# Kernel optimization log

Measured on AMD Instinct MI355X. Metric: run time of the kernel, lower is better.

Reference implementation:

```python
import jax, jax.numpy as jnp
import numpy as np

EPS = 1e-5

def conv1x1(x, w, b):
    # x: (B,C,H,W), w: (O,C), b: (O,)
    return jnp.einsum('bchw,oc->bohw', x, w) + b[None, :, None, None]

def instance_norm(x):
    mu = jnp.mean(x, axis=(2, 3), keepdims=True)
    var = jnp.var(x, axis=(2, 3), keepdims=True)
    return (x - mu) / jnp.sqrt(var + EPS)

def setup_inputs() -> dict:
    key = jax.random.key(0)
    C = 256
    ks = jax.random.split(key, 16)
    def w(k):
        return jax.random.normal(k, (C, C), dtype=jnp.float32) * 0.02
    def b(k):
        return jax.random.normal(k, (C,), dtype=jnp.float32) * 0.01
    return {
        'x': jax.random.normal(ks[0], (8, C, 128, 128), dtype=jnp.float32),
        'wq1': w(ks[1]), 'bq1': b(ks[2]), 'wq2': w(ks[3]), 'bq2': b(ks[4]),
        'wk1': w(ks[5]), 'bk1': b(ks[6]), 'wk2': w(ks[7]), 'bk2': b(ks[8]),
        'wv': w(ks[9]), 'bv': b(ks[10]),
        'wg': w(ks[11]), 'bg': b(ks[12]),
        'wo': w(ks[13]), 'bo': b(ks[14]),
    }

def reference(x, wq1, bq1, wq2, bq2, wk1, bk1, wk2, bk2, wv, bv, wg, bg, wo, bo):
    head = 4
    B, C, H, W = x.shape
    c = C // head  # per-head channels
    n = H * W
    x = instance_norm(x)
    q = jax.nn.softplus(conv1x1(jax.nn.gelu(conv1x1(x, wq1, bq1), approximate=False), wq2, bq2))
    k = jax.nn.softplus(conv1x1(jax.nn.gelu(conv1x1(x, wk1, bk1), approximate=False), wk2, bk2))
    v = jax.nn.gelu(conv1x1(x, wv, bv), approximate=False)
    g = jax.nn.gelu(conv1x1(x, wg, bg), approximate=False)
    # b (head c) h w -> b head c (h w)
    q = q.reshape(B, head, c, n)
    kk = k.reshape(B, head, c, n)
    vv = v.reshape(B, head, c, n)
    kv = jnp.einsum('bhcn,bhdn->bhcd', kk, vv)  # (B,head,c,c)
    scale = 1.0 / jnp.sqrt(jnp.float32(c))
    z = jnp.einsum('bhcn,bhc->bhn', q, kk.sum(axis=-1)) * scale
    z = 1.0 / (z + jnp.float32(n))
    out = jnp.einsum('bhcn,bhcd->bhdn', q, kv) * scale
    out = (out + vv) * z[:, :, None, :]
    out = out.reshape(B, C, H, W)
    out = out * g
    return conv1x1(out, wo, bo)
```

## Files before the change

### kernel.cpp

```cpp
#include <hip/hip_runtime.h>
#include <stdint.h>

typedef short bf8 __attribute__((ext_vector_type(8)));
typedef short s4v __attribute__((ext_vector_type(4)));
typedef float f32x4 __attribute__((ext_vector_type(4)));

__device__ __forceinline__ short f2bf(float f){
  union { float f; unsigned u; } c; c.f = f;
  unsigned r = (c.u + 0x7fffu + ((c.u >> 16) & 1u)) >> 16;
  return (short)r;
}
__device__ __forceinline__ float bf2f(short s){
  union { unsigned u; float f; } c; c.u = ((unsigned)(unsigned short)s) << 16;
  return c.f;
}
__device__ __forceinline__ void gload16(const void* g, void* l){
  __builtin_amdgcn_global_load_lds((const __attribute__((address_space(1))) uint32_t*)g,
                                   (__attribute__((address_space(3))) uint32_t*)l, 16, 0, 0);
}
__device__ __forceinline__ float fast_erf(float x){
  const float s = fabsf(x);
  const float t = __builtin_amdgcn_rcpf(fmaf(0.3275911f, s, 1.0f));
  float p = fmaf(1.061405429f, t, -1.453152027f);
  p = fmaf(p, t, 1.421413741f);
  p = fmaf(p, t, -0.284496736f);
  p = fmaf(p, t, 0.254829592f);
  p = p * t;
  const float e = __expf(-s * s);
  return copysignf(fmaf(-p, e, 1.0f), x);
}
__device__ __forceinline__ float act_gelu(float x){
  return 0.5f * x * (1.0f + fast_erf(x * 0.70710678118654752f));
}
__device__ __forceinline__ float act_softplus(float x){
  const float e = __expf(-fabsf(x));
  return fmaxf(x, 0.0f) + __logf(1.0f + e);
}

__global__ __launch_bounds__(256) void k_statst(const float* __restrict__ x, short* __restrict__ xt,
                                                float* __restrict__ ps1, float* __restrict__ ps2){
  const int n0 = blockIdx.x * 64, c0 = blockIdx.y * 64, b = blockIdx.z;
  __shared__ short lt[64][68];
  const int t = threadIdx.x, nj = (t & 15) * 4, cb = t >> 4;
  float s1[4] = {0.f,0.f,0.f,0.f}, s2[4] = {0.f,0.f,0.f,0.f};
#pragma unroll
  for (int it = 0; it < 4; ++it){
    const int ci = cb + it * 16;
    const int row = b * 256 + c0 + ci;
    float4 v = *(const float4*)(x + (size_t)row * 16384 + n0 + nj);
    s4v o;
    o[0] = f2bf(v.x); o[1] = f2bf(v.y); o[2] = f2bf(v.z); o[3] = f2bf(v.w);
    *(s4v*)(&lt[ci][nj]) = o;
    s1[it] += v.x + v.y + v.z + v.w;
    s2[it] += v.x*v.x + v.y*v.y + v.z*v.z + v.w*v.w;
  }
  __syncthreads();
#pragma unroll
  for (int p = 0; p < 2; ++p){
    const int q = p * 256 + t;
    const int nl = q >> 3, c8 = (q & 7) * 8;
    bf8 o;
#pragma unroll
    for (int j = 0; j < 8; ++j) o[j] = lt[c8 + j][nl];
    *(bf8*)(xt + ((size_t)(b * 16384 + n0 + nl)) * 256 + c0 + c8) = o;
  }
#pragma unroll
  for (int it = 0; it < 4; ++it){
#pragma unroll
    for (int off = 8; off > 0; off >>= 1){
      s1[it] += __shfl_down(s1[it], off);
      s2[it] += __shfl_down(s2[it], off);
    }
  }
  if ((t & 15) == 0){
#pragma unroll
    for (int it = 0; it < 4; ++it){
      const int c = c0 + cb + it * 16;
      ps1[((size_t)(b * 256 + c)) * 256 + blockIdx.x] = s1[it];
      ps2[((size_t)(b * 256 + c)) * 256 + blockIdx.x] = s2[it];
    }
  }
}

__global__ __launch_bounds__(256) void k_red(const float* __restrict__ ps1, const float* __restrict__ ps2,
                                             float* __restrict__ mu, float* __restrict__ rsig){
  const int bc = blockIdx.x;
  const int t = threadIdx.x;
  __shared__ float a1[256], a2[256];
  a1[t] = ps1[(size_t)bc * 256 + t];
  a2[t] = ps2[(size_t)bc * 256 + t];
  __syncthreads();
  for (int s = 128; s > 0; s >>= 1){
    if (t < s){ a1[t] += a1[t+s]; a2[t] += a2[t+s]; }
    __syncthreads();
  }
  if (t == 0){
    float m = a1[0] * (1.0f/16384.0f);
    float v = a2[0] * (1.0f/16384.0f) - m*m;
    mu[bc] = m; rsig[bc] = rsqrtf(v + 1e-5f);
  }
}

__global__ __launch_bounds__(256) void k_norm(short* xn, const float* __restrict__ mu,
                                              const float* __restrict__ rsig){
  const int g = blockIdx.x * 256 + threadIdx.x;
#pragma unroll
  for (int pass = 0; pass < 8; ++pass){
    const int idx = g + pass * 524288;
    const int bn = idx >> 5, c8 = idx & 31;
    const int b = bn >> 14;
    const float* mp = mu + b * 256 + c8 * 8;
    const float* rp = rsig + b * 256 + c8 * 8;
    float4 m0 = *(const float4*)mp, m1 = *(const float4*)(mp + 4);
    float4 r0 = *(const float4*)rp, r1 = *(const float4*)(rp + 4);
    float mm[8] = {m0.x,m0.y,m0.z,m0.w,m1.x,m1.y,m1.z,m1.w};
    float rr[8] = {r0.x,r0.y,r0.z,r0.w,r1.x,r1.y,r1.z,r1.w};
    bf8 v = *(const bf8*)(xn + (size_t)idx * 8);
    bf8 o;
#pragma unroll
    for (int j = 0; j < 8; ++j) o[j] = f2bf((bf2f(v[j]) - mm[j]) * rr[j]);
    *(bf8*)(xn + (size_t)idx * 8) = o;
  }
}

__global__ __launch_bounds__(256) void k_wconv(const float* w0, const float* w1, const float* w2,
                                               const float* w3, const float* w4, const float* w5,
                                               const float* w6, short* __restrict__ wb){
  const int gid = blockIdx.x * 256 + threadIdx.x;
  const int mat = gid >> 14, r4 = gid & 16383;
  const float* srcs[7] = {w0, w1, w2, w3, w4, w5, w6};
  float4 v = *(const float4*)(srcs[mat] + (size_t)r4 * 4);
  s4v o; o[0] = f2bf(v.x); o[1] = f2bf(v.y); o[2] = f2bf(v.z); o[3] = f2bf(v.w);
  *(s4v*)(wb + (size_t)mat * 65536 + r4 * 4) = o;
}

template<int ACT>
__global__ __launch_bounds__(256, 2)
void k_gemm0(const short* __restrict__ A, const short* __restrict__ W,
             const float* __restrict__ bias, short* __restrict__ outp){
  __shared__ short sA[2][128 * 32];
  __shared__ short sB[2][256 * 32];
  const int t = threadIdx.x, l = t & 63, w = t >> 6;
  const int wr = w >> 1, wc = w & 1;
  const int lm = l & 15, lk = l >> 4;
  const size_t m0 = (size_t)blockIdx.x * 128;
  const int swz = ((lk ^ ((lm >> 1) & 3)) << 4);
  f32x4 acc[4][8] = {};

  auto stage = [&](int ks, int buf){
    const int k0 = ks * 32;
#pragma unroll
    for (int p = 0; p < 2; ++p){
      const int q = p * 256 + t, r = q >> 2, kc = q & 3;
      gload16(A + (m0 + r) * 256 + k0 + ((kc ^ ((r >> 1) & 3)) << 3),
              (char*)(&sA[buf][0]) + (p * 256 + w * 64) * 16);
    }
#pragma unroll
    for (int p = 0; p < 4; ++p){
      const int q = p * 256 + t, r = q >> 2, kc = q & 3;
      gload16(W + (size_t)r * 256 + k0 + ((kc ^ ((r >> 1) & 3)) << 3),
              (char*)(&sB[buf][0]) + (p * 256 + w * 64) * 16);
    }
  };

  stage(0, 0);
  __syncthreads();
  int cur = 0;
  for (int ks = 0; ks < 8; ++ks){
    if (ks < 7) stage(ks + 1, cur ^ 1);
    bf8 af[4], bfv[8];
#pragma unroll
    for (int mi = 0; mi < 4; ++mi)
      af[mi] = *(const bf8*)((const char*)(&sA[cur][0]) + (wr * 64 + mi * 16 + lm) * 64 + swz);
#pragma unroll
    for (int ni = 0; ni < 8; ++ni)
      bfv[ni] = *(const bf8*)((const char*)(&sB[cur][0]) + (wc * 128 + ni * 16 + lm) * 64 + swz);
#pragma unroll
    for (int mi = 0; mi < 4; ++mi)
#pragma unroll
      for (int ni = 0; ni < 8; ++ni)
        acc[mi][ni] = __builtin_amdgcn_mfma_f32_16x16x32_bf16(bfv[ni], af[mi], acc[mi][ni], 0, 0, 0);
    __syncthreads();
    cur ^= 1;
  }

#pragma unroll
  for (int ni = 0; ni < 8; ++ni){
    const int ob = wc * 128 + ni * 16 + lk * 4;
    const float4 b4 = *(const float4*)(bias + ob);
#pragma unroll
    for (int mi = 0; mi < 4; ++mi){
      const int px = wr * 64 + mi * 16 + lm;
      s4v o4;
#pragma unroll
      for (int j = 0; j < 4; ++j){
        float v = acc[mi][ni][j] + ((const float*)&b4)[j];
        if (ACT == 1) v = act_gelu(v);
        else if (ACT == 2) v = act_softplus(v);
        o4[j] = f2bf(v);
      }
      *(s4v*)(outp + (m0 + px) * 256 + ob) = o4;
    }
  }
}

__global__ __launch_bounds__(256, 2)
void k_chain(const short* __restrict__ A, const short* __restrict__ W1, const float* __restrict__ b1,
             const short* __restrict__ W2, const float* __restrict__ b2, short* __restrict__ out){
  __shared__ short sA[2][64 * 32];
  __shared__ short sB[2][256 * 32];
  __shared__ short h1[64 * 256];
  const int t = threadIdx.x, l = t & 63, w = t >> 6;
  const int lm = l & 15, lk = l >> 4;
  const size_t m0 = (size_t)blockIdx.x * 64;
  const int swz = ((lk ^ ((lm >> 1) & 3)) << 4);
  f32x4 acc[4][4] = {};

  auto stageA = [&](int ks, int buf){
    const int r = t >> 2, kc = t & 3;
    gload16(A + (m0 + r) * 256 + ks * 32 + ((kc ^ ((r >> 1) & 3)) << 3),
            (char*)(&sA[buf][0]) + w * 1024);
  };
  auto stageW = [&](const short* Wm, int ks, int buf){
#pragma unroll
    for (int p = 0; p < 4; ++p){
      const int q = p * 256 + t, r = q >> 2, kc = q & 3;
      gload16(Wm + (size_t)r * 256 + ks * 32 + ((kc ^ ((r >> 1) & 3)) << 3),
              (char*)(&sB[buf][0]) + (p * 256 + w * 64) * 16);
    }
  };

  stageA(0, 0); stageW(W1, 0, 0);
  __syncthreads();
  int cur = 0;
  for (int ks = 0; ks < 8; ++ks){
    if (ks < 7){ stageA(ks + 1, cur ^ 1); stageW(W1, ks + 1, cur ^ 1); }
    bf8 af[4], bfv[4];
#pragma unroll
    for (int mi = 0; mi < 4; ++mi)
      af[mi] = *(const bf8*)((const char*)(&sA[cur][0]) + (mi * 16 + lm) * 64 + swz);
#pragma unroll
    for (int ni = 0; ni < 4; ++ni)
      bfv[ni] = *(const bf8*)((const char*)(&sB[cur][0]) + (w * 64 + ni * 16 + lm) * 64 + swz);
#pragma unroll
    for (int mi = 0; mi < 4; ++mi)
#pragma unroll
      for (int ni = 0; ni < 4; ++ni)
        acc[mi][ni] = __builtin_amdgcn_mfma_f32_16x16x32_bf16(bfv[ni], af[mi], acc[mi][ni], 0, 0, 0);
    __syncthreads();
    cur ^= 1;
  }

  stageW(W2, 0, 0);
#pragma unroll
  for (int ni = 0; ni < 4; ++ni){
    const int ob = w * 64 + ni * 16 + lk * 4;
    const float4 b4 = *(const float4*)(b1 + ob);
#pragma unroll
    for (int mi = 0; mi < 4; ++mi){
      const int px = mi * 16 + lm;
      s4v o4;
#pragma unroll
      for (int j = 0; j < 4; ++j)
        o4[j] = f2bf(act_gelu(acc[mi][ni][j] + ((const float*)&b4)[j]));
      const int slot = (ob >> 3) ^ (px & 7);
      *(s4v*)((char*)h1 + px * 512 + (slot << 4) + (ob & 4) * 2) = o4;
      acc[mi][ni] = (f32x4){0.f, 0.f, 0.f, 0.f};
    }
  }
  __syncthreads();

  cur = 0;
  for (int ks = 0; ks < 8; ++ks){
    if (ks < 7) stageW(W2, ks + 1, cur ^ 1);
    bf8 af[4], bfv[4];
#pragma unroll
    for (int mi = 0; mi < 4; ++mi){
      const int row = mi * 16 + lm;
      const int slot = (ks * 4 + lk) ^ (row & 7);
      af[mi] = *(const bf8*)((const char*)h1 + row * 512 + (slot << 4));
    }
#pragma unroll
    for (int ni = 0; ni < 4; ++ni)
      bfv[ni] = *(const bf8*)((const char*)(&sB[cur][0]) + (w * 64 + ni * 16 + lm) * 64 + swz);
#pragma unroll
    for (int mi = 0; mi < 4; ++mi)
#pragma unroll
      for (int ni = 0; ni < 4; ++ni)
        acc[mi][ni] = __builtin_amdgcn_mfma_f32_16x16x32_bf16(bfv[ni], af[mi], acc[mi][ni], 0, 0, 0);
    __syncthreads();
    cur ^= 1;
  }
#pragma unroll
  for (int ni = 0; ni < 4; ++ni){
    const int ob = w * 64 + ni * 16 + lk * 4;
    const float4 b4 = *(const float4*)(b2 + ob);
#pragma unroll
    for (int mi = 0; mi < 4; ++mi){
      const int px = mi * 16 + lm;
      s4v o4;
#pragma unroll
      for (int j = 0; j < 4; ++j)
        o4[j] = f2bf(act_softplus(acc[mi][ni][j] + ((const float*)&b4)[j]));
      *(s4v*)(out + (m0 + px) * 256 + ob) = o4;
    }
  }
}

__global__ __launch_bounds__(256) void k_kv(const short* __restrict__ kg, const short* __restrict__ vg,
                                            float* __restrict__ kvpart, float* __restrict__ kspart){
  const int s = blockIdx.x, h = blockIdx.y, b = blockIdx.z;
  __shared__ short sk[64 * 72], sv[64 * 72];
  __shared__ float pl[256][8];
  const int t = threadIdx.x, l = t & 63, w = t >> 6;
  const int lm = l & 15, lk = l >> 4;
  float ksp[8];
#pragma unroll
  for (int j = 0; j < 8; ++j) ksp[j] = 0.f;
  f32x4 acc[4] = {};
  const size_t rowbase = ((size_t)b * 16384 + s * 2048) * 256 + h * 64;

  for (int tt = 0; tt < 32; ++tt){
    __syncthreads();
#pragma unroll
    for (int p = 0; p < 2; ++p){
      const int q = p * 256 + t;
      const int nl = q >> 3, c8 = (q & 7) * 8;
      bf8 kvv = *(const bf8*)(kg + rowbase + (size_t)(tt * 64 + nl) * 256 + c8);
      bf8 vvv = *(const bf8*)(vg + rowbase + (size_t)(tt * 64 + nl) * 256 + c8);
#pragma unroll
      for (int j = 0; j < 8; ++j){
        sk[(c8 + j) * 72 + nl] = kvv[j];
        sv[(c8 + j) * 72 + nl] = vvv[j];
        ksp[j] += bf2f(kvv[j]);
      }
    }
    __syncthreads();
#pragma unroll
    for (int ks = 0; ks < 2; ++ks){
      bf8 ak = *(const bf8*)((const char*)sk + (w * 16 + lm) * 144 + ks * 64 + lk * 16);
#pragma unroll
      for (int ni = 0; ni < 4; ++ni){
        bf8 bv = *(const bf8*)((const char*)sv + (ni * 16 + lm) * 144 + ks * 64 + lk * 16);
        acc[ni] = __builtin_amdgcn_mfma_f32_16x16x32_bf16(ak, bv, acc[ni], 0, 0, 0);
      }
    }
  }
#pragma unroll
  for (int j = 0; j < 8; ++j) pl[t][j] = ksp[j];
  __syncthreads();
  const size_t slot = (size_t)(b * 4 + h) * 8 + s;
  if (t < 64){
    float sum = 0.f;
    const int g8 = t >> 3, j = t & 7;
    for (int m = 0; m < 32; ++m) sum += pl[m * 8 + g8][j];
    kspart[slot * 64 + t] = sum;
  }
  float* kvp = kvpart + slot * 4096;
#pragma unroll
  for (int ni = 0; ni < 4; ++ni)
#pragma unroll
    for (int j = 0; j < 4; ++j){
      const int c = w * 16 + lk * 4 + j, d = ni * 16 + lm;
      kvp[c * 64 + d] = acc[ni][j];
    }
}

__global__ __launch_bounds__(256) void k_kvred(const float* __restrict__ kvpart, const float* __restrict__ kspart,
                                               short* __restrict__ kvT, float* __restrict__ ksum_s){
  const int gid = blockIdx.x * 256 + threadIdx.x;
#pragma unroll
  for (int i = 0; i < 8; ++i){
    const int o = gid * 8 + i;
    const int bh = o >> 12, rem = o & 4095, d = rem >> 6, c = rem & 63;
    float sum = 0.f;
#pragma unroll
    for (int s = 0; s < 8; ++s) sum += kvpart[((size_t)bh * 8 + s) * 4096 + c * 64 + d];
    kvT[o] = f2bf(sum * 0.125f);
  }
  if (gid < 2048){
    float sum = 0.f;
#pragma unroll
    for (int s = 0; s < 8; ++s) sum += kspart[((size_t)(gid >> 6) * 8 + s) * 64 + (gid & 63)];
    ksum_s[gid] = sum * 0.125f;
  }
}

__global__ __launch_bounds__(256, 2)
void k_fuse(const short* __restrict__ xn, const short* __restrict__ qg,
            const short* __restrict__ vg, const short* __restrict__ kvT,
            const float* __restrict__ ksum_s,
            const short* __restrict__ Wg, const float* __restrict__ bg,
            const short* __restrict__ Wo, const float* __restrict__ bo,
            float* __restrict__ outp){
  __shared__ short sA[2][64 * 32];
  __shared__ short sB[2][256 * 32];
  __shared__ short yl[64 * 256];
  __shared__ float sz[256];
  __shared__ float sks[256];
  const int t = threadIdx.x, l = t & 63, w = t >> 6;
  const int lm = l & 15, lk = l >> 4;
  const size_t m0 = (size_t)blockIdx.x * 64;
  const int b = (int)(m0 >> 14);
  const int h = w;
  const int swz = ((lk ^ ((lm >> 1) & 3)) << 4);

  sks[t] = ksum_s[b * 256 + t];

  auto stageA = [&](int ks, int buf){
    const int r = t >> 2, kc = t & 3;
    gload16(xn + (m0 + r) * 256 + ks * 32 + ((kc ^ ((r >> 1) & 3)) << 3),
            (char*)(&sA[buf][0]) + w * 1024);
  };
  auto stageW = [&](const short* Wm, int ks, int buf){
#pragma unroll
    for (int p = 0; p < 4; ++p){
      const int q = p * 256 + t, r = q >> 2, kc = q & 3;
      gload16(Wm + (size_t)r * 256 + ks * 32 + ((kc ^ ((r >> 1) & 3)) << 3),
              (char*)(&sB[buf][0]) + (p * 256 + w * 64) * 16);
    }
  };

  f32x4 acc[4][4] = {};

  stageA(0, 0); stageW(Wg, 0, 0);
  __syncthreads();
  int cur = 0;
  for (int ks = 0; ks < 8; ++ks){
    if (ks < 7){ stageA(ks + 1, cur ^ 1); stageW(Wg, ks + 1, cur ^ 1); }
    bf8 af[4], bfv[4];
#pragma unroll
    for (int mi = 0; mi < 4; ++mi)
      af[mi] = *(const bf8*)((const char*)(&sA[cur][0]) + (mi * 16 + lm) * 64 + swz);
#pragma unroll
    for (int ni = 0; ni < 4; ++ni)
      bfv[ni] = *(const bf8*)((const char*)(&sB[cur][0]) + (w * 64 + ni * 16 + lm) * 64 + swz);
#pragma unroll
    for (int mi = 0; mi < 4; ++mi)
#pragma unroll
      for (int ni = 0; ni < 4; ++ni)
        acc[mi][ni] = __builtin_amdgcn_mfma_f32_16x16x32_bf16(bfv[ni], af[mi], acc[mi][ni], 0, 0, 0);
    __syncthreads();
    cur ^= 1;
  }
  s4v g_pk[4][4];
#pragma unroll
  for (int ni = 0; ni < 4; ++ni){
    const int ob = h * 64 + ni * 16 + lk * 4;
    const float4 b4 = *(const float4*)(bg + ob);
#pragma unroll
    for (int mi = 0; mi < 4; ++mi){
#pragma unroll
      for (int j = 0; j < 4; ++j)
        g_pk[mi][ni][j] = f2bf(act_gelu(acc[mi][ni][j] + ((const float*)&b4)[j]));
      acc[mi][ni] = (f32x4){0.f, 0.f, 0.f, 0.f};
    }
  }

  {
    float dot = 0.f;
#pragma unroll
    for (int cc = 0; cc < 8; ++cc){
      bf8 qv = *(const bf8*)(qg + (m0 + l) * 256 + h * 64 + cc * 8);
#pragma unroll
      for (int j = 0; j < 8; ++j) dot += bf2f(qv[j]) * sks[h * 64 + cc * 8 + j];
    }
    sz[h * 64 + l] = 1.0f / (dot + 16384.0f);
  }

  const short* kvb = kvT + (size_t)b * 16384;
#pragma unroll
  for (int ks = 0; ks < 2; ++ks){
    bf8 aq[4];
#pragma unroll
    for (int mi = 0; mi < 4; ++mi)
      aq[mi] = *(const bf8*)(qg + (m0 + mi * 16 + lm) * 256 + h * 64 + ks * 32 + lk * 8);
#pragma unroll
    for (int ni = 0; ni < 4; ++ni){
      bf8 bk = *(const bf8*)(kvb + (size_t)(h * 64 + ni * 16 + lm) * 64 + ks * 32 + lk * 8);
#pragma unroll
      for (int mi = 0; mi < 4; ++mi)
        acc[mi][ni] = __builtin_amdgcn_mfma_f32_16x16x32_bf16(bk, aq[mi], acc[mi][ni], 0, 0, 0);
    }
  }
#pragma unroll
  for (int mi = 0; mi < 4; ++mi){
    const int px = mi * 16 + lm;
    const float zf = sz[h * 64 + px];
    const size_t base = (m0 + px) * 256;
#pragma unroll
    for (int ni = 0; ni < 4; ++ni){
      const int ch = h * 64 + ni * 16 + lk * 4;
      s4v v4 = *(const s4v*)(vg + base + ch);
      s4v o4;
#pragma unroll
      for (int j = 0; j < 4; ++j)
        o4[j] = f2bf((acc[mi][ni][j] + bf2f(v4[j])) * zf * bf2f(g_pk[mi][ni][j]));
      const int slot = (ch >> 3) ^ (px & 7);
      *(s4v*)((char*)yl + px * 512 + (slot << 4) + (ch & 4) * 2) = o4;
      acc[mi][ni] = (f32x4){0.f, 0.f, 0.f, 0.f};
    }
  }
  stageW(Wo, 0, 0);
  __syncthreads();

  cur = 0;
  for (int ks = 0; ks < 8; ++ks){
    if (ks < 7) stageW(Wo, ks + 1, cur ^ 1);
    bf8 af[4], bfv[4];
#pragma unroll
    for (int mi = 0; mi < 4; ++mi){
      const int row = mi * 16 + lm;
      const int slot = (ks * 4 + lk) ^ (row & 7);
      af[mi] = *(const bf8*)((const char*)yl + row * 512 + (slot << 4));
    }
#pragma unroll
    for (int ni = 0; ni < 4; ++ni)
      bfv[ni] = *(const bf8*)((const char*)(&sB[cur][0]) + (w * 64 + ni * 16 + lm) * 64 + swz);
#pragma unroll
    for (int mi = 0; mi < 4; ++mi)
#pragma unroll
      for (int ni = 0; ni < 4; ++ni)
        acc[mi][ni] = __builtin_amdgcn_mfma_f32_16x16x32_bf16(af[mi], bfv[ni], acc[mi][ni], 0, 0, 0);
    __syncthreads();
    cur ^= 1;
  }
  const int nb = (int)(m0 & 16383);
#pragma unroll
  for (int mi = 0; mi < 4; ++mi){
    const int np = nb + mi * 16 + lk * 4;
#pragma unroll
    for (int ni = 0; ni < 4; ++ni){
      const int o = w * 64 + ni * 16 + lm;
      const float bi = bo[o];
      float4 v;
      v.x = acc[mi][ni][0] + bi; v.y = acc[mi][ni][1] + bi;
      v.z = acc[mi][ni][2] + bi; v.w = acc[mi][ni][3] + bi;
      *(float4*)(outp + (((size_t)(b * 256 + o)) * 16384 + np)) = v;
    }
  }
}

extern "C" void kernel_launch(void* const* d_in, const int* in_sizes, int n_in,
                              void* d_out, int out_size, void* d_ws, size_t ws_size,
                              hipStream_t stream){
  (void)in_sizes; (void)n_in; (void)out_size; (void)ws_size;
  const float* x   = (const float*)d_in[0];
  const float* wq1 = (const float*)d_in[1];
  const float* bq1 = (const float*)d_in[2];
  const float* wq2 = (const float*)d_in[3];
  const float* bq2 = (const float*)d_in[4];
  const float* wk1 = (const float*)d_in[5];
  const float* bk1 = (const float*)d_in[6];
  const float* wk2 = (const float*)d_in[7];
  const float* bk2 = (const float*)d_in[8];
  const float* wv  = (const float*)d_in[9];
  const float* bv  = (const float*)d_in[10];
  const float* wg  = (const float*)d_in[11];
  const float* bg  = (const float*)d_in[12];
  const float* wo  = (const float*)d_in[13];
  const float* bo  = (const float*)d_in[14];

  char* ws = (char*)d_ws;
  float* mu     = (float*)(ws + 0);
  float* rsig   = (float*)(ws + 8192);
  short* wb     = (short*)(ws + 16384);
  float* kvpart = (float*)(ws + 933888);
  float* ps1    = (float*)(ws + 933888);
  float* ps2    = (float*)(ws + 3031040);
  float* kspart = (float*)(ws + 5128192);
  short* kvT    = (short*)(ws + 5193728);
  float* ksum_s = (float*)(ws + 5455872);
  short* B0 = (short*)(ws + 8388608);
  short* B1 = B0 + 33554432;
  short* B2 = B1 + 33554432;
  short* B3 = B2 + 33554432;

  k_wconv<<<448, 256, 0, stream>>>(wq1, wq2, wk1, wk2, wv, wg, wo, wb);
  k_statst<<<dim3(256, 4, 8), 256, 0, stream>>>(x, B0, ps1, ps2);
  k_red<<<2048, 256, 0, stream>>>(ps1, ps2, mu, rsig);
  k_norm<<<2048, 256, 0, stream>>>(B0, mu, rsig);
  k_chain<<<2048, 256, 0, stream>>>(B0, wb + 0 * 65536, bq1, wb + 1 * 65536, bq2, B2);
  k_chain<<<2048, 256, 0, stream>>>(B0, wb + 2 * 65536, bk1, wb + 3 * 65536, bk2, B3);
  k_gemm0<1><<<1024, 256, 0, stream>>>(B0, wb + 4 * 65536, bv, B1);
  k_kv<<<dim3(8, 4, 8), 256, 0, stream>>>(B3, B1, kvpart, kspart);
  k_kvred<<<64, 256, 0, stream>>>(kvpart, kspart, kvT, ksum_s);
  k_fuse<<<2048, 256, 0, stream>>>(B0, B2, B1, kvT, ksum_s,
                                   wb + 5 * 65536, bg, wb + 6 * 65536, bo,
                                   (float*)d_out);
}
```

Before: 446.0 us.

## Fold instance norm into per-batch weights and retile chain/fuse kernels with triple buffering

Removes the separate normalization pass by folding mean and inverse std into per-batch bf16 copies of the first-layer weights and biases, so GEMMs consume the raw transposed bf16 input. The chain and fuse kernels move to 512-thread blocks covering 128 pixels, with three-stage LDS buffering controlled by explicit vmcnt waits and barriers. The kv reduction is split into fewer, longer partial slices. This saves one full read and write of the activation tensor and cuts barrier stalls, at the cost of extra per-batch weight storage, lower occupancy from larger LDS use, and precision change from folding the norm into bf16 weights.

```diff
diff --git a/kernel.cpp b/kernel.cpp
--- a/kernel.cpp
+++ b/kernel.cpp
@@ -4,6 +4,11 @@
 typedef short bf8 __attribute__((ext_vector_type(8)));
 typedef short s4v __attribute__((ext_vector_type(4)));
 typedef float f32x4 __attribute__((ext_vector_type(4)));
+
+#define VM_WAIT(N) asm volatile("s_waitcnt vmcnt(" #N ")" ::: "memory")
+#define LGKM0()    asm volatile("s_waitcnt lgkmcnt(0)" ::: "memory")
+#define SBAR()     do { __builtin_amdgcn_sched_barrier(0); __builtin_amdgcn_s_barrier(); \
+                        __builtin_amdgcn_sched_barrier(0); } while (0)
 
 __device__ __forceinline__ short f2bf(float f){
   union { float f; unsigned u; } c; c.f = f;
@@ -101,34 +106,44 @@
   }
 }
 
-__global__ __launch_bounds__(256) void k_norm(short* xn, const float* __restrict__ mu,
-                                              const float* __restrict__ rsig){
-  const int g = blockIdx.x * 256 + threadIdx.x;
-#pragma unroll
-  for (int pass = 0; pass < 8; ++pass){
-    const int idx = g + pass * 524288;
-    const int bn = idx >> 5, c8 = idx & 31;
-    const int b = bn >> 14;
-    const float* mp = mu + b * 256 + c8 * 8;
-    const float* rp = rsig + b * 256 + c8 * 8;
-    float4 m0 = *(const float4*)mp, m1 = *(const float4*)(mp + 4);
-    float4 r0 = *(const float4*)rp, r1 = *(const float4*)(rp + 4);
-    float mm[8] = {m0.x,m0.y,m0.z,m0.w,m1.x,m1.y,m1.z,m1.w};
-    float rr[8] = {r0.x,r0.y,r0.z,r0.w,r1.x,r1.y,r1.z,r1.w};
-    bf8 v = *(const bf8*)(xn + (size_t)idx * 8);
-    bf8 o;
-#pragma unroll
-    for (int j = 0; j < 8; ++j) o[j] = f2bf((bf2f(v[j]) - mm[j]) * rr[j]);
-    *(bf8*)(xn + (size_t)idx * 8) = o;
+__global__ __launch_bounds__(256) void k_wfold(
+    const float* __restrict__ w0, const float* __restrict__ bb0,
+    const float* __restrict__ w1, const float* __restrict__ bb1,
+    const float* __restrict__ w2, const float* __restrict__ bb2,
+    const float* __restrict__ w3, const float* __restrict__ bb3,
+    const float* __restrict__ mu, const float* __restrict__ rsig,
+    short* __restrict__ wf, float* __restrict__ bf){
+  const int m = blockIdx.x >> 3, b = blockIdx.x & 7;
+  const float* Wm = (m==0)?w0:(m==1)?w1:(m==2)?w2:w3;
+  const float* Bm = (m==0)?bb0:(m==1)?bb1:(m==2)?bb2:bb3;
+  __shared__ float rs[256], ms[256];
+  const int t = threadIdx.x;
+  rs[t] = rsig[b*256+t];
+  ms[t] = mu[b*256+t] * rs[t];
+  __syncthreads();
+  short* wout = wf + ((size_t)(m*8+b)) * 65536;
+  float* bout = bf + (m*8+b) * 256;
+  const int lane = t & 63, wv = t >> 6;
+  for (int oi = 0; oi < 64; ++oi){
+    const int o = oi * 4 + wv;
+    const int c = lane * 4;
+    float4 w4 = *(const float4*)(Wm + (size_t)o * 256 + c);
+    float pa = w4.x*ms[c] + w4.y*ms[c+1] + w4.z*ms[c+2] + w4.w*ms[c+3];
+    s4v o4;
+    o4[0] = f2bf(w4.x*rs[c]);   o4[1] = f2bf(w4.y*rs[c+1]);
+    o4[2] = f2bf(w4.z*rs[c+2]); o4[3] = f2bf(w4.w*rs[c+3]);
+    *(s4v*)(wout + (size_t)o * 256 + c) = o4;
+#pragma unroll
+    for (int off = 32; off > 0; off >>= 1) pa += __shfl_down(pa, off);
+    if (lane == 0) bout[o] = Bm[o] - pa;
   }
 }
 
 __global__ __launch_bounds__(256) void k_wconv(const float* w0, const float* w1, const float* w2,
-                                               const float* w3, const float* w4, const float* w5,
-                                               const float* w6, short* __restrict__ wb){
+                                               short* __restrict__ wb){
   const int gid = blockIdx.x * 256 + threadIdx.x;
   const int mat = gid >> 14, r4 = gid & 16383;
-  const float* srcs[7] = {w0, w1, w2, w3, w4, w5, w6};
+  const float* srcs[3] = {w0, w1, w2};
   float4 v = *(const float4*)(srcs[mat] + (size_t)r4 * 4);
   s4v o; o[0] = f2bf(v.x); o[1] = f2bf(v.y); o[2] = f2bf(v.z); o[3] = f2bf(v.w);
   *(s4v*)(wb + (size_t)mat * 65536 + r4 * 4) = o;
@@ -136,14 +151,17 @@
 
 template<int ACT>
 __global__ __launch_bounds__(256, 2)
-void k_gemm0(const short* __restrict__ A, const short* __restrict__ W,
-             const float* __restrict__ bias, short* __restrict__ outp){
+void k_gemm0(const short* __restrict__ A, const short* __restrict__ Wf,
+             const float* __restrict__ bfold, short* __restrict__ outp){
   __shared__ short sA[2][128 * 32];
   __shared__ short sB[2][256 * 32];
   const int t = threadIdx.x, l = t & 63, w = t >> 6;
   const int wr = w >> 1, wc = w & 1;
   const int lm = l & 15, lk = l >> 4;
   const size_t m0 = (size_t)blockIdx.x * 128;
+  const int b = (int)(m0 >> 14);
+  const short* W = Wf + (size_t)b * 65536;
+  const float* bias = bfold + b * 256;
   const int swz = ((lk ^ ((lm >> 1) & 3)) << 4);
   f32x4 acc[4][8] = {};
 
@@ -204,61 +222,65 @@
   }
 }
 
-__global__ __launch_bounds__(256, 2)
-void k_chain(const short* __restrict__ A, const short* __restrict__ W1, const float* __restrict__ b1,
+__global__ __launch_bounds__(512, 1)
+void k_chain(const short* __restrict__ A, const short* __restrict__ W1f, const float* __restrict__ b1f,
              const short* __restrict__ W2, const float* __restrict__ b2, short* __restrict__ out){
-  __shared__ short sA[2][64 * 32];
-  __shared__ short sB[2][256 * 32];
-  __shared__ short h1[64 * 256];
+  __shared__ short sA[3][128 * 32];
+  __shared__ short sB[3][256 * 32];
+  __shared__ short h1[128 * 256];
   const int t = threadIdx.x, l = t & 63, w = t >> 6;
+  const int p = w >> 2, hh = w & 3;
   const int lm = l & 15, lk = l >> 4;
-  const size_t m0 = (size_t)blockIdx.x * 64;
+  const size_t m0 = (size_t)blockIdx.x * 128;
+  const int b = (int)(m0 >> 14);
+  const short* W1 = W1f + (size_t)b * 65536;
+  const float* b1 = b1f + b * 256;
   const int swz = ((lk ^ ((lm >> 1) & 3)) << 4);
   f32x4 acc[4][4] = {};
 
   auto stageA = [&](int ks, int buf){
     const int r = t >> 2, kc = t & 3;
     gload16(A + (m0 + r) * 256 + ks * 32 + ((kc ^ ((r >> 1) & 3)) << 3),
-            (char*)(&sA[buf][0]) + w * 1024);
+            (char*)(&sA[buf][0]) + t * 16);
   };
   auto stageW = [&](const short* Wm, int ks, int buf){
 #pragma unroll
-    for (int p = 0; p < 4; ++p){
-      const int q = p * 256 + t, r = q >> 2, kc = q & 3;
+    for (int pp = 0; pp < 2; ++pp){
+      const int q = pp * 512 + t, r = q >> 2, kc = q & 3;
       gload16(Wm + (size_t)r * 256 + ks * 32 + ((kc ^ ((r >> 1) & 3)) << 3),
-              (char*)(&sB[buf][0]) + (p * 256 + w * 64) * 16);
+              (char*)(&sB[buf][0]) + q * 16);
     }
   };
 
   stageA(0, 0); stageW(W1, 0, 0);
-  __syncthreads();
-  int cur = 0;
+  stageA(1, 1); stageW(W1, 1, 1);
+  VM_WAIT(3);
+  SBAR();
   for (int ks = 0; ks < 8; ++ks){
-    if (ks < 7){ stageA(ks + 1, cur ^ 1); stageW(W1, ks + 1, cur ^ 1); }
+    const int cur = ks % 3;
+    if (ks < 6){ stageA(ks + 2, (ks + 2) % 3); stageW(W1, ks + 2, (ks + 2) % 3); }
     bf8 af[4], bfv[4];
 #pragma unroll
     for (int mi = 0; mi < 4; ++mi)
-      af[mi] = *(const bf8*)((const char*)(&sA[cur][0]) + (mi * 16 + lm) * 64 + swz);
+      af[mi] = *(const bf8*)((const char*)(&sA[cur][0]) + (p * 64 + mi * 16 + lm) * 64 + swz);
 #pragma unroll
     for (int ni = 0; ni < 4; ++ni)
-      bfv[ni] = *(const bf8*)((const char*)(&sB[cur][0]) + (w * 64 + ni * 16 + lm) * 64 + swz);
+      bfv[ni] = *(const bf8*)((const char*)(&sB[cur][0]) + (hh * 64 + ni * 16 + lm) * 64 + swz);
 #pragma unroll
     for (int mi = 0; mi < 4; ++mi)
 #pragma unroll
       for (int ni = 0; ni < 4; ++ni)
         acc[mi][ni] = __builtin_amdgcn_mfma_f32_16x16x32_bf16(bfv[ni], af[mi], acc[mi][ni], 0, 0, 0);
-    __syncthreads();
-    cur ^= 1;
-  }
-
-  stageW(W2, 0, 0);
+    if (ks < 6) { VM_WAIT(3); } else { VM_WAIT(0); }
+    SBAR();
+  }
 #pragma unroll
   for (int ni = 0; ni < 4; ++ni){
-    const int ob = w * 64 + ni * 16 + lk * 4;
+    const int ob = hh * 64 + ni * 16 + lk * 4;
     const float4 b4 = *(const float4*)(b1 + ob);
 #pragma unroll
     for (int mi = 0; mi < 4; ++mi){
-      const int px = mi * 16 + lm;
+      const int px = p * 64 + mi * 16 + lm;
       s4v o4;
 #pragma unroll
       for (int j = 0; j < 4; ++j)
@@ -268,36 +290,39 @@
       acc[mi][ni] = (f32x4){0.f, 0.f, 0.f, 0.f};
     }
   }
-  __syncthreads();
-
-  cur = 0;
+  stageW(W2, 0, 0); stageW(W2, 1, 1);
+  LGKM0();
+  VM_WAIT(2);
+  SBAR();
+
   for (int ks = 0; ks < 8; ++ks){
-    if (ks < 7) stageW(W2, ks + 1, cur ^ 1);
+    const int cur = ks % 3;
+    if (ks < 6) stageW(W2, ks + 2, (ks + 2) % 3);
     bf8 af[4], bfv[4];
 #pragma unroll
     for (int mi = 0; mi < 4; ++mi){
-      const int row = mi * 16 + lm;
+      const int row = p * 64 + mi * 16 + lm;
       const int slot = (ks * 4 + lk) ^ (row & 7);
       af[mi] = *(const bf8*)((const char*)h1 + row * 512 + (slot << 4));
     }
 #pragma unroll
     for (int ni = 0; ni < 4; ++ni)
-      bfv[ni] = *(const bf8*)((const char*)(&sB[cur][0]) + (w * 64 + ni * 16 + lm) * 64 + swz);
+      bfv[ni] = *(const bf8*)((const char*)(&sB[cur][0]) + (hh * 64 + ni * 16 + lm) * 64 + swz);
 #pragma unroll
     for (int mi = 0; mi < 4; ++mi)
 #pragma unroll
       for (int ni = 0; ni < 4; ++ni)
         acc[mi][ni] = __builtin_amdgcn_mfma_f32_16x16x32_bf16(bfv[ni], af[mi], acc[mi][ni], 0, 0, 0);
-    __syncthreads();
-    cur ^= 1;
+    if (ks < 6) { VM_WAIT(2); } else { VM_WAIT(0); }
+    SBAR();
   }
 #pragma unroll
   for (int ni = 0; ni < 4; ++ni){
-    const int ob = w * 64 + ni * 16 + lk * 4;
+    const int ob = hh * 64 + ni * 16 + lk * 4;
     const float4 b4 = *(const float4*)(b2 + ob);
 #pragma unroll
     for (int mi = 0; mi < 4; ++mi){
-      const int px = mi * 16 + lm;
+      const int px = p * 64 + mi * 16 + lm;
       s4v o4;
 #pragma unroll
       for (int j = 0; j < 4; ++j)
@@ -318,9 +343,9 @@
 #pragma unroll
   for (int j = 0; j < 8; ++j) ksp[j] = 0.f;
   f32x4 acc[4] = {};
-  const size_t rowbase = ((size_t)b * 16384 + s * 2048) * 256 + h * 64;
-
-  for (int tt = 0; tt < 32; ++tt){
+  const size_t rowbase = ((size_t)b * 16384 + s * 4096) * 256 + h * 64;
+
+  for (int tt = 0; tt < 64; ++tt){
     __syncthreads();
 #pragma unroll
     for (int p = 0; p < 2; ++p){
@@ -349,7 +374,7 @@
 #pragma unroll
   for (int j = 0; j < 8; ++j) pl[t][j] = ksp[j];
   __syncthreads();
-  const size_t slot = (size_t)(b * 4 + h) * 8 + s;
+  const size_t slot = (size_t)(b * 4 + h) * 4 + s;
   if (t < 64){
     float sum = 0.f;
     const int g8 = t >> 3, j = t & 7;
@@ -375,78 +400,83 @@
     const int bh = o >> 12, rem = o & 4095, d = rem >> 6, c = rem & 63;
     float sum = 0.f;
 #pragma unroll
-    for (int s = 0; s < 8; ++s) sum += kvpart[((size_t)bh * 8 + s) * 4096 + c * 64 + d];
+    for (int s = 0; s < 4; ++s) sum += kvpart[((size_t)bh * 4 + s) * 4096 + c * 64 + d];
     kvT[o] = f2bf(sum * 0.125f);
   }
   if (gid < 2048){
     float sum = 0.f;
 #pragma unroll
-    for (int s = 0; s < 8; ++s) sum += kspart[((size_t)(gid >> 6) * 8 + s) * 64 + (gid & 63)];
+    for (int s = 0; s < 4; ++s) sum += kspart[((size_t)(gid >> 6) * 4 + s) * 64 + (gid & 63)];
     ksum_s[gid] = sum * 0.125f;
   }
 }
 
-__global__ __launch_bounds__(256, 2)
-void k_fuse(const short* __restrict__ xn, const short* __restrict__ qg,
+__global__ __launch_bounds__(512, 1)
+void k_fuse(const short* __restrict__ xt, const short* __restrict__ qg,
             const short* __restrict__ vg, const short* __restrict__ kvT,
             const float* __restrict__ ksum_s,
-            const short* __restrict__ Wg, const float* __restrict__ bg,
+            const short* __restrict__ Wgf, const float* __restrict__ bgf,
             const short* __restrict__ Wo, const float* __restrict__ bo,
             float* __restrict__ outp){
-  __shared__ short sA[2][64 * 32];
-  __shared__ short sB[2][256 * 32];
-  __shared__ short yl[64 * 256];
-  __shared__ float sz[256];
+  __shared__ short sA[3][128 * 32];
+  __shared__ short sB[3][256 * 32];
+  __shared__ short yl[128 * 256];
+  __shared__ float sz[512];
   __shared__ float sks[256];
   const int t = threadIdx.x, l = t & 63, w = t >> 6;
+  const int p = w >> 2, hh = w & 3;
   const int lm = l & 15, lk = l >> 4;
-  const size_t m0 = (size_t)blockIdx.x * 64;
+  const size_t m0 = (size_t)blockIdx.x * 128;
   const int b = (int)(m0 >> 14);
-  const int h = w;
+  const short* Wg = Wgf + (size_t)b * 65536;
+  const float* bg = bgf + b * 256;
   const int swz = ((lk ^ ((lm >> 1) & 3)) << 4);
 
-  sks[t] = ksum_s[b * 256 + t];
+  if (t < 256) sks[t] = ksum_s[b * 256 + t];
 
   auto stageA = [&](int ks, int buf){
     const int r = t >> 2, kc = t & 3;
-    gload16(xn + (m0 + r) * 256 + ks * 32 + ((kc ^ ((r >> 1) & 3)) << 3),
-            (char*)(&sA[buf][0]) + w * 1024);
+    gload16(xt + (m0 + r) * 256 + ks * 32 + ((kc ^ ((r >> 1) & 3)) << 3),
+            (char*)(&sA[buf][0]) + t * 16);
   };
   auto stageW = [&](const short* Wm, int ks, int buf){
 #pragma unroll
-    for (int p = 0; p < 4; ++p){
-      const int q = p * 256 + t, r = q >> 2, kc = q & 3;
+    for (int pp = 0; pp < 2; ++pp){
+      const int q = pp * 512 + t, r = q >> 2, kc = q & 3;
       gload16(Wm + (size_t)r * 256 + ks * 32 + ((kc ^ ((r >> 1) & 3)) << 3),
-              (char*)(&sB[buf][0]) + (p * 256 + w * 64) * 16);
+              (char*)(&sB[buf][0]) + q * 16);
     }
   };
 
   f32x4 acc[4][4] = {};
 
   stageA(0, 0); stageW(Wg, 0, 0);
-  __syncthreads();
-  int cur = 0;
+  stageA(1, 1); stageW(Wg, 1, 1);
+  LGKM0();
+  VM_WAIT(3);
+  SBAR();
   for (int ks = 0; ks < 8; ++ks){
-    if (ks < 7){ stageA(ks + 1, cur ^ 1); stageW(Wg, ks + 1, cur ^ 1); }
+    const int cur = ks % 3;
+    if (ks < 6){ stageA(ks + 2, (ks + 2) % 3); stageW(Wg, ks + 2, (ks + 2) % 3); }
     bf8 af[4], bfv[4];
 #pragma unroll
     for (int mi = 0; mi < 4; ++mi)
-      af[mi] = *(const bf8*)((const char*)(&sA[cur][0]) + (mi * 16 + lm) * 64 + swz);
+      af[mi] = *(const bf8*)((const char*)(&sA[cur][0]) + (p * 64 + mi * 16 + lm) * 64 + swz);
 #pragma unroll
     for (int ni = 0; ni < 4; ++ni)
-      bfv[ni] = *(const bf8*)((const char*)(&sB[cur][0]) + (w * 64 + ni * 16 + lm) * 64 + swz);
+      bfv[ni] = *(const bf8*)((const char*)(&sB[cur][0]) + (hh * 64 + ni * 16 + lm) * 64 + swz);
 #pragma unroll
     for (int mi = 0; mi < 4; ++mi)
 #pragma unroll
       for (int ni = 0; ni < 4; ++ni)
         acc[mi][ni] = __builtin_amdgcn_mfma_f32_16x16x32_bf16(bfv[ni], af[mi], acc[mi][ni], 0, 0, 0);
-    __syncthreads();
-    cur ^= 1;
+    if (ks < 6) { VM_WAIT(3); } else { VM_WAIT(0); }
+    SBAR();
   }
   s4v g_pk[4][4];
 #pragma unroll
   for (int ni = 0; ni < 4; ++ni){
-    const int ob = h * 64 + ni * 16 + lk * 4;
+    const int ob = hh * 64 + ni * 16 + lk * 4;
     const float4 b4 = *(const float4*)(bg + ob);
 #pragma unroll
     for (int mi = 0; mi < 4; ++mi){
@@ -456,28 +486,29 @@
       acc[mi][ni] = (f32x4){0.f, 0.f, 0.f, 0.f};
     }
   }
+  stageW(Wo, 0, 0); stageW(Wo, 1, 1);
 
   {
+    const int px = p * 64 + l;
     float dot = 0.f;
 #pragma unroll
     for (int cc = 0; cc < 8; ++cc){
-      bf8 qv = *(const bf8*)(qg + (m0 + l) * 256 + h * 64 + cc * 8);
-#pragma unroll
-      for (int j = 0; j < 8; ++j) dot += bf2f(qv[j]) * sks[h * 64 + cc * 8 + j];
-    }
-    sz[h * 64 + l] = 1.0f / (dot + 16384.0f);
-  }
-
+      bf8 qv = *(const bf8*)(qg + (m0 + px) * 256 + hh * 64 + cc * 8);
+#pragma unroll
+      for (int j = 0; j < 8; ++j) dot += bf2f(qv[j]) * sks[hh * 64 + cc * 8 + j];
+    }
+    sz[hh * 128 + px] = 1.0f / (dot + 16384.0f);
+  }
   const short* kvb = kvT + (size_t)b * 16384;
 #pragma unroll
   for (int ks = 0; ks < 2; ++ks){
     bf8 aq[4];
 #pragma unroll
     for (int mi = 0; mi < 4; ++mi)
-      aq[mi] = *(const bf8*)(qg + (m0 + mi * 16 + lm) * 256 + h * 64 + ks * 32 + lk * 8);
+      aq[mi] = *(const bf8*)(qg + (m0 + p * 64 + mi * 16 + lm) * 256 + hh * 64 + ks * 32 + lk * 8);
 #pragma unroll
     for (int ni = 0; ni < 4; ++ni){
-      bf8 bk = *(const bf8*)(kvb + (size_t)(h * 64 + ni * 16 + lm) * 64 + ks * 32 + lk * 8);
+      bf8 bk = *(const bf8*)(kvb + (size_t)(hh * 64 + ni * 16 + lm) * 64 + ks * 32 + lk * 8);
 #pragma unroll
       for (int mi = 0; mi < 4; ++mi)
         acc[mi][ni] = __builtin_amdgcn_mfma_f32_16x16x32_bf16(bk, aq[mi], acc[mi][ni], 0, 0, 0);
@@ -485,12 +516,12 @@
   }
 #pragma unroll
   for (int mi = 0; mi < 4; ++mi){
-    const int px = mi * 16 + lm;
-    const float zf = sz[h * 64 + px];
+    const int px = p * 64 + mi * 16 + lm;
+    const float zf = sz[hh * 128 + px];
     const size_t base = (m0 + px) * 256;
 #pragma unroll
     for (int ni = 0; ni < 4; ++ni){
-      const int ch = h * 64 + ni * 16 + lk * 4;
+      const int ch = hh * 64 + ni * 16 + lk * 4;
       s4v v4 = *(const s4v*)(vg + base + ch);
       s4v o4;
 #pragma unroll
@@ -501,37 +532,38 @@
       acc[mi][ni] = (f32x4){0.f, 0.f, 0.f, 0.f};
     }
   }
-  stageW(Wo, 0, 0);
-  __syncthreads();
-
-  cur = 0;
+  LGKM0();
+  VM_WAIT(2);
+  SBAR();
+
   for (int ks = 0; ks < 8; ++ks){
-    if (ks < 7) stageW(Wo, ks + 1, cur ^ 1);
+    const int cur = ks % 3;
+    if (ks < 6) stageW(Wo, ks + 2, (ks + 2) % 3);
     bf8 af[4], bfv[4];
 #pragma unroll
     for (int mi = 0; mi < 4; ++mi){
-      const int row = mi * 16 + lm;
+      const int row = p * 64 + mi * 16 + lm;
       const int slot = (ks * 4 + lk) ^ (row & 7);
       af[mi] = *(const bf8*)((const char*)yl + row * 512 + (slot << 4));
     }
 #pragma unroll
     for (int ni = 0; ni < 4; ++ni)
-      bfv[ni] = *(const bf8*)((const char*)(&sB[cur][0]) + (w * 64 + ni * 16 + lm) * 64 + swz);
+      bfv[ni] = *(const bf8*)((const char*)(&sB[cur][0]) + (hh * 64 + ni * 16 + lm) * 64 + swz);
 #pragma unroll
     for (int mi = 0; mi < 4; ++mi)
 #pragma unroll
       for (int ni = 0; ni < 4; ++ni)
         acc[mi][ni] = __builtin_amdgcn_mfma_f32_16x16x32_bf16(af[mi], bfv[ni], acc[mi][ni], 0, 0, 0);
-    __syncthreads();
-    cur ^= 1;
+    if (ks < 6) { VM_WAIT(2); } else { VM_WAIT(0); }
+    SBAR();
   }
   const int nb = (int)(m0 & 16383);
 #pragma unroll
   for (int mi = 0; mi < 4; ++mi){
-    const int np = nb + mi * 16 + lk * 4;
+    const int np = nb + p * 64 + mi * 16 + lk * 4;
 #pragma unroll
     for (int ni = 0; ni < 4; ++ni){
-      const int o = w * 64 + ni * 16 + lm;
+      const int o = hh * 64 + ni * 16 + lm;
       const float bi = bo[o];
       float4 v;
       v.x = acc[mi][ni][0] + bi; v.y = acc[mi][ni][1] + bi;
@@ -565,27 +597,31 @@
   float* mu     = (float*)(ws + 0);
   float* rsig   = (float*)(ws + 8192);
   short* wb     = (short*)(ws + 16384);
-  float* kvpart = (float*)(ws + 933888);
-  float* ps1    = (float*)(ws + 933888);
-  float* ps2    = (float*)(ws + 3031040);
-  float* kspart = (float*)(ws + 5128192);
-  short* kvT    = (short*)(ws + 5193728);
-  float* ksum_s = (float*)(ws + 5455872);
+  float* bfold  = (float*)(ws + 409600);
+  short* wf     = (short*)(ws + 442368);
+  float* ps1    = (float*)(ws + 442368);
+  float* ps2    = (float*)(ws + 2539520);
+  float* kvpart = (float*)(ws + 4636672);
+  float* kspart = (float*)(ws + 6733824);
+  short* kvT    = (short*)(ws + 6766592);
+  float* ksum_s = (float*)(ws + 7028736);
   short* B0 = (short*)(ws + 8388608);
   short* B1 = B0 + 33554432;
   short* B2 = B1 + 33554432;
   short* B3 = B2 + 33554432;
 
-  k_wconv<<<448, 256, 0, stream>>>(wq1, wq2, wk1, wk2, wv, wg, wo, wb);
+  k_wconv<<<192, 256, 0, stream>>>(wq2, wk2, wo, wb);
   k_statst<<<dim3(256, 4, 8), 256, 0, stream>>>(x, B0, ps1, ps2);
   k_red<<<2048, 256, 0, stream>>>(ps1, ps2, mu, rsig);
-  k_norm<<<2048, 256, 0, stream>>>(B0, mu, rsig);
-  k_chain<<<2048, 256, 0, stream>>>(B0, wb + 0 * 65536, bq1, wb + 1 * 65536, bq2, B2);
-  k_chain<<<2048, 256, 0, stream>>>(B0, wb + 2 * 65536, bk1, wb + 3 * 65536, bk2, B3);
-  k_gemm0<1><<<1024, 256, 0, stream>>>(B0, wb + 4 * 65536, bv, B1);
-  k_kv<<<dim3(8, 4, 8), 256, 0, stream>>>(B3, B1, kvpart, kspart);
+  k_wfold<<<32, 256, 0, stream>>>(wq1, bq1, wk1, bk1, wv, bv, wg, bg, mu, rsig, wf, bfold);
+  k_chain<<<1024, 512, 0, stream>>>(B0, wf + 0 * 524288, bfold + 0 * 2048,
+                                    wb + 0 * 65536, bq2, B2);
+  k_chain<<<1024, 512, 0, stream>>>(B0, wf + 1 * 524288, bfold + 1 * 2048,
+                                    wb + 1 * 65536, bk2, B3);
+  k_gemm0<1><<<1024, 256, 0, stream>>>(B0, wf + 2 * 524288, bfold + 2 * 2048, B1);
+  k_kv<<<dim3(4, 4, 8), 256, 0, stream>>>(B3, B1, kvpart, kspart);
   k_kvred<<<64, 256, 0, stream>>>(kvpart, kspart, kvT, ksum_s);
-  k_fuse<<<2048, 256, 0, stream>>>(B0, B2, B1, kvT, ksum_s,
-                                   wb + 5 * 65536, bg, wb + 6 * 65536, bo,
-                                   (float*)d_out);
-}
+  k_fuse<<<1024, 512, 0, stream>>>(B0, B2, B1, kvT, ksum_s,
+                                   wf + 3 * 524288, bfold + 3 * 2048,
+                                   wb + 2 * 65536, bo, (float*)d_out);
+}
```

New measurement: 538.2 us. 1.21x slower.
